# Kernel tuning notes

Measured on AMD Instinct MI355X. Metric: run time of the kernel, lower is better.

## Reference

```python
import jax, jax.numpy as jnp
import numpy as np

B, S, H = 2, 4096, 1024   # batch, seq, hidden_size
I = 512                    # moe_intermediate_size
E = 8                      # n_routed_experts
TOPK = 2                   # num_experts_per_tok
NGROUP = 2                 # n_group
TOPK_GROUP = 1             # topk_group
ROUTED_SCALE = 1.0         # routed_scaling_factor


def setup_inputs() -> dict:
    key = jax.random.key(0)
    ks = jax.random.split(key, 9)
    def w(k, shape, s=0.05):
        return jax.random.normal(k, shape, dtype=jnp.float32) * s
    return {
        "hidden_states": jax.random.normal(ks[0], (B, S, H), dtype=jnp.float32),
        "router_weight": w(ks[1], (E, H)),
        "correction_bias": w(ks[2], (E,)),
        "w_gate": w(ks[3], (E, H, I)),
        "w_up": w(ks[4], (E, H, I)),
        "w_down": w(ks[5], (E, I, H)),
        "sw_gate": w(ks[6], (H, I)),
        "sw_up": w(ks[7], (H, I)),
        "sw_down": w(ks[8], (I, H)),
    }


def _silu(x):
    return x * jax.nn.sigmoid(x)


def reference(hidden_states, router_weight, correction_bias,
              w_gate, w_up, w_down, sw_gate, sw_up, sw_down):
    b, s, h = hidden_states.shape
    x = hidden_states.reshape(-1, h)                       # [T, H]

    # ---- Glm4MoeTopkRouter (sigmoid scores + group top-k) ----
    logits = x @ router_weight.T                            # [T, E] (fp32)
    scores = jax.nn.sigmoid(logits)
    scores_for_choice = scores + correction_bias[None, :]
    e_per_g = E // NGROUP
    # group score = sum of top-2 biased scores within each group
    group_scores = jax.lax.top_k(
        scores_for_choice.reshape(-1, NGROUP, e_per_g), 2)[0].sum(-1)  # [T, G]
    group_idx = jax.lax.top_k(group_scores, TOPK_GROUP)[1]             # [T, Gk]
    group_mask = jax.nn.one_hot(group_idx, NGROUP, dtype=scores.dtype).sum(1)  # [T, G]
    score_mask = jnp.repeat(group_mask, e_per_g, axis=1)               # [T, E]
    masked = jnp.where(score_mask > 0, scores_for_choice, 0.0)
    topk_idx = jax.lax.top_k(masked, TOPK)[1]                          # [T, K]
    topk_w = jnp.take_along_axis(scores, topk_idx, axis=1)             # [T, K]
    topk_w = topk_w / (topk_w.sum(-1, keepdims=True) + 1e-20)          # norm_topk_prob
    topk_w = topk_w * ROUTED_SCALE

    # ---- routed experts: gated-SiLU MLP per expert, weighted combine ----
    # combine weights [T, E]: zero for unselected experts (exactly equals the
    # original per-expert gather/scatter sum)
    comb = (jax.nn.one_hot(topk_idx, E, dtype=x.dtype) * topk_w[..., None]).sum(1)
    g = jnp.einsum('th,ehi->tei', x, w_gate)               # [T, E, I]
    u = jnp.einsum('th,ehi->tei', x, w_up)
    y = jnp.einsum('tei,eih->teh', _silu(g) * u, w_down)   # [T, E, H]
    routed = jnp.einsum('teh,te->th', y, comb).reshape(b, s, h)

    # ---- shared experts on the residual ----
    shared = (_silu(hidden_states @ sw_gate) * (hidden_states @ sw_up)) @ sw_down
    return routed + shared
```

## Files before the change

### kernel.cpp

```cpp
#include <hip/hip_runtime.h>
#include <math.h>
#include <stdint.h>

#define T_TOK 8192
#define HDIM 1024
#define IDIM 512
#define NEXP 8
#define NGRP 2
#define EPG 4

typedef unsigned short u16;
typedef __attribute__((ext_vector_type(8))) short short8;
typedef __attribute__((ext_vector_type(4))) float f32x4;

#define GLD16(gp, lp) __builtin_amdgcn_global_load_lds(                        \
    (const __attribute__((address_space(1))) unsigned int*)(gp),               \
    (__attribute__((address_space(3))) unsigned int*)(lp), 16, 0, 0)

__device__ __forceinline__ u16 f2bf(float f) {
    unsigned int u = __float_as_uint(f);
    u += 0x7fffu + ((u >> 16) & 1u);
    return (u16)(u >> 16);
}
__device__ __forceinline__ float bf2f(u16 v) {
    return __uint_as_float(((unsigned int)v) << 16);
}

__global__ __launch_bounds__(256)
void prologue(const float* __restrict__ X,
              const float* __restrict__ Wr, const float* __restrict__ bias,
              u16* __restrict__ Xb, float* __restrict__ wpair, int* __restrict__ topk_ids,
              const float* __restrict__ wg,  const float* __restrict__ wu,
              const float* __restrict__ wdn, const float* __restrict__ swg,
              const float* __restrict__ swu, const float* __restrict__ swd,
              u16* __restrict__ wgT, u16* __restrict__ wuT, u16* __restrict__ wdnT,
              u16* __restrict__ swgT, u16* __restrict__ swuT, u16* __restrict__ swdT)
{
    __shared__ float tile[64][65];
    const int bid = blockIdx.x;

    if (bid < 2048) {
        int wave = threadIdx.x >> 6;
        int lane = threadIdx.x & 63;
        int t = bid * 4 + wave;

        float acc[NEXP];
#pragma unroll
        for (int e = 0; e < NEXP; ++e) acc[e] = 0.f;

        const float4* X4 = (const float4*)(X + (size_t)t * HDIM);
#pragma unroll
        for (int jj = 0; jj < 4; ++jj) {
            float4 xv = X4[lane + jj * 64];
            ushort4 bv;
            bv.x = f2bf(xv.x); bv.y = f2bf(xv.y); bv.z = f2bf(xv.z); bv.w = f2bf(xv.w);
            *(ushort4*)(Xb + (size_t)t * HDIM + (size_t)(lane + jj * 64) * 4) = bv;
#pragma unroll
            for (int e = 0; e < NEXP; ++e) {
                const float4* W4 = (const float4*)(Wr + (size_t)e * HDIM);
                float4 wv = W4[lane + jj * 64];
                acc[e] += xv.x * wv.x + xv.y * wv.y + xv.z * wv.z + xv.w * wv.w;
            }
        }
#pragma unroll
        for (int e = 0; e < NEXP; ++e) {
#pragma unroll
            for (int off = 32; off >= 1; off >>= 1)
                acc[e] += __shfl_xor(acc[e], off, 64);
        }

        if (lane == 0) {
            float s[NEXP], b[NEXP];
#pragma unroll
            for (int e = 0; e < NEXP; ++e) {
                s[e] = 1.f / (1.f + expf(-acc[e]));
                b[e] = s[e] + bias[e];
            }
            float gs[NGRP];
#pragma unroll
            for (int g = 0; g < NGRP; ++g) {
                float m1 = -1e30f, m2 = -1e30f;
#pragma unroll
                for (int j = 0; j < EPG; ++j) {
                    float v = b[g * EPG + j];
                    if (v > m1) { m2 = m1; m1 = v; }
                    else if (v > m2) { m2 = v; }
                }
                gs[g] = m1 + m2;
            }
            int bg = (gs[1] > gs[0]) ? 1 : 0;
            float masked[NEXP];
#pragma unroll
            for (int e = 0; e < NEXP; ++e)
                masked[e] = ((e >> 2) == bg) ? b[e] : 0.0f;
            int i0 = 0; float v0 = masked[0];
#pragma unroll
            for (int e = 1; e < NEXP; ++e)
                if (masked[e] > v0) { v0 = masked[e]; i0 = e; }
            int i1 = -1; float v1 = -1e30f;
#pragma unroll
            for (int e = 0; e < NEXP; ++e) {
                if (e == i0) continue;
                if (masked[e] > v1) { v1 = masked[e]; i1 = e; }
            }
            float w0 = s[i0], w1 = s[i1];
            float inv = 1.f / (w0 + w1 + 1e-20f);
            w0 *= inv; w1 *= inv;
            wpair[t * 2 + 0] = w0;
            wpair[t * 2 + 1] = w1;
            topk_ids[t] = i0 | (i1 << 8);
        }
        return;
    }

    int tb = bid - 2048;
    int m = tb >> 7;
    int i = tb & 127;
    const float* src; u16* dst; int R, C;
    const size_t EW = (size_t)HDIM * IDIM;
    if (m < 8)       { src = wg  + (size_t)m * EW;        dst = wgT  + (size_t)m * EW;        R = HDIM; C = IDIM; }
    else if (m < 16) { src = wu  + (size_t)(m - 8) * EW;  dst = wuT  + (size_t)(m - 8) * EW;  R = HDIM; C = IDIM; }
    else if (m < 24) { src = wdn + (size_t)(m - 16) * EW; dst = wdnT + (size_t)(m - 16) * EW; R = IDIM; C = HDIM; }
    else if (m == 24){ src = swg; dst = swgT; R = HDIM; C = IDIM; }
    else if (m == 25){ src = swu; dst = swuT; R = HDIM; C = IDIM; }
    else             { src = swd; dst = swdT; R = IDIM; C = HDIM; }
    int r0, c0;
    if (R == HDIM) { r0 = (i & 15) * 64; c0 = (i >> 4) * 64; }
    else           { r0 = (i & 7) * 64;  c0 = (i >> 3) * 64; }

    int t = threadIdx.x;
    int row = t >> 2;
#pragma unroll
    for (int j = 0; j < 4; ++j) {
        int c = ((t & 3) + j * 4) * 4;
        *(float4*)&tile[row][c] = *(const float4*)(src + (size_t)(r0 + row) * C + c0 + c);
    }
    __syncthreads();
    int c = t >> 2;
    int rchunk = (t & 3) * 16;
    __attribute__((aligned(16))) u16 pack[16];
#pragma unroll
    for (int k = 0; k < 16; ++k)
        pack[k] = f2bf(tile[rchunk + k][c]);
    uint4* d4 = (uint4*)(dst + (size_t)(c0 + c) * R + r0 + rchunk);
    d4[0] = *(uint4*)&pack[0];
    d4[1] = *(uint4*)&pack[8];
}

__global__ __launch_bounds__(256)
void build_lists(const int* __restrict__ topk_ids,
                 int* __restrict__ counts,
                 int* __restrict__ pair_id)
{
    const int e = blockIdx.x;
    const int tid = threadIdx.x;
    const int lane = tid & 63;
    const int wid = tid >> 6;
    __shared__ int wsum[4];
    __shared__ int rb;
    if (tid == 0) rb = 0;
    __syncthreads();

    int* dst = pair_id + e * T_TOK;
    for (int c0 = 0; c0 < T_TOK; c0 += 256) {
        int t = c0 + tid;
        int ids = topk_ids[t];
        bool m0 = (ids & 0xff) == e;
        bool m1 = ((ids >> 8) & 0xff) == e;
        unsigned long long b0 = __ballot(m0);
        unsigned long long b1 = __ballot(m1);
        int n0 = __popcll(b0);
        int n1 = __popcll(b1);
        if (lane == 0) wsum[wid] = n0 + n1;
        __syncthreads();
        int pre = 0, tot = 0;
#pragma unroll
        for (int w = 0; w < 4; ++w) {
            int v = wsum[w];
            if (w < wid) pre += v;
            tot += v;
        }
        int mybase = rb + pre;
        unsigned long long ltmask = (lane == 63) ? ~0ull >> 1 : ((1ull << lane) - 1);
        if (m0) dst[mybase + __popcll(b0 & ltmask)] = t * 2;
        if (m1) dst[mybase + n0 + __popcll(b1 & ltmask)] = t * 2 + 1;
        __syncthreads();
        if (tid == 0) rb += tot;
    }
    __syncthreads();
    if (tid == 0) counts[e] = rb;
}

__global__ __launch_bounds__(512)
void gateup_all(const u16* __restrict__ Xb,
                const u16* __restrict__ WgT, const u16* __restrict__ WuT,
                const u16* __restrict__ sWgT, const u16* __restrict__ sWuT,
                u16* __restrict__ hs,
                u16* __restrict__ hp,
                const int* __restrict__ counts,
                const int* __restrict__ pair_id)
{
    const int z = blockIdx.z;
    const bool SH = (z == 0);
    const int e = z - 1;
    const int nrows = SH ? T_TOK : counts[e];
    const int bm0 = blockIdx.y * 128;
    if (bm0 >= nrows) return;
    const int bn0 = blockIdx.x * 64;
    const u16* wgT = SH ? sWgT : WgT + (size_t)e * HDIM * IDIM;
    const u16* wuT = SH ? sWuT : WuT + (size_t)e * HDIM * IDIM;
    const int* plist = SH ? nullptr : (pair_id + e * T_TOK);
    u16* hout = SH ? hs : hp;

    int ebase = 0;
    if (!SH) {
#pragma unroll
        for (int i = 0; i < NEXP; ++i) ebase += (i < e) ? counts[i] : 0;
    }

    __shared__ __attribute__((aligned(16))) short As[128 * 64];
    __shared__ __attribute__((aligned(16))) short Bg[64 * 64];
    __shared__ __attribute__((aligned(16))) short Bu[64 * 64];

    const int tid = threadIdx.x;
    const int lane = tid & 63;
    const int wid = tid >> 6;

    const char* aptr[2];
#pragma unroll
    for (int i = 0; i < 2; ++i) {
        int g = wid * 2 + i;
        int r = g * 8 + (lane >> 3);
        int row = bm0 + r;
        int srow;
        if (SH) srow = row;
        else    srow = (row < nrows) ? (plist[row] >> 1) : 0;
        int cslot = ((lane & 7) ^ (r & 7)) * 8;
        aptr[i] = (const char*)(Xb + (size_t)srow * HDIM + cslot);
    }
    const char* bgptr; const char* buptr;
    {
        int r = wid * 8 + (lane >> 3);
        int nn = bn0 + r;
        int cslot = ((lane & 7) ^ (r & 7)) * 8;
        bgptr = (const char*)(wgT + (size_t)nn * HDIM + cslot);
        buptr = (const char*)(wuT + (size_t)nn * HDIM + cslot);
    }

    const int wm = wid & 3, wn = wid >> 2;
    const int m0 = wm * 32, n0 = wn * 32;
    const int lr = lane & 15, lg = lane >> 4;

    f32x4 accg[2][2] = {};
    f32x4 accu[2][2] = {};

    for (int k0 = 0; k0 < HDIM; k0 += 64) {
#pragma unroll
        for (int i = 0; i < 2; ++i) {
            GLD16(aptr[i], (char*)As + (wid * 2 + i) * 1024);
            aptr[i] += 128;
        }
        GLD16(bgptr, (char*)Bg + wid * 1024);
        GLD16(buptr, (char*)Bu + wid * 1024);
        bgptr += 128; buptr += 128;
        __syncthreads();
#pragma unroll
        for (int kk = 0; kk < 2; ++kk) {
            short8 af[2], bgf[2], buf_[2];
#pragma unroll
            for (int mf = 0; mf < 2; ++mf) {
                int row = m0 + mf * 16 + lr;
                int slot = (kk * 4 + lg) ^ (row & 7);
                af[mf] = *(const short8*)((const char*)As + row * 128 + slot * 16);
            }
#pragma unroll
            for (int nf = 0; nf < 2; ++nf) {
                int row = n0 + nf * 16 + lr;
                int slot = (kk * 4 + lg) ^ (row & 7);
                bgf[nf]  = *(const short8*)((const char*)Bg + row * 128 + slot * 16);
                buf_[nf] = *(const short8*)((const char*)Bu + row * 128 + slot * 16);
            }
#pragma unroll
            for (int mf = 0; mf < 2; ++mf)
#pragma unroll
                for (int nf = 0; nf < 2; ++nf) {
                    accg[mf][nf] = __builtin_amdgcn_mfma_f32_16x16x32_bf16(af[mf], bgf[nf],  accg[mf][nf], 0, 0, 0);
                    accu[mf][nf] = __builtin_amdgcn_mfma_f32_16x16x32_bf16(af[mf], buf_[nf], accu[mf][nf], 0, 0, 0);
                }
        }
        __syncthreads();
    }

#pragma unroll
    for (int mf = 0; mf < 2; ++mf) {
#pragma unroll
        for (int j = 0; j < 4; ++j) {
            int row = bm0 + m0 + mf * 16 + lg * 4 + j;
            if (row >= nrows) continue;
            int outrow = SH ? row : (ebase + row);
            u16* dst = hout + (size_t)outrow * IDIM + bn0 + n0 + lr;
#pragma unroll
            for (int nf = 0; nf < 2; ++nf) {
                float g = accg[mf][nf][j], u = accu[mf][nf][j];
                float sg = g / (1.f + __expf(-g));
                dst[nf * 16] = f2bf(sg * u);
            }
        }
    }
}

__global__ __launch_bounds__(512)
void down_routed(const u16* __restrict__ Hp,
                 const u16* __restrict__ WdT,
                 u16* __restrict__ y0,
                 u16* __restrict__ y1,
                 const float* __restrict__ wpair,
                 const int* __restrict__ counts,
                 const int* __restrict__ pair_id)
{
    const int e = blockIdx.z;
    const int nrows = counts[e];
    const int bm0 = blockIdx.y * 128;
    if (bm0 >= nrows) return;
    const int bn0 = blockIdx.x * 128;
    const u16* wdT = WdT + (size_t)e * HDIM * IDIM;
    const int* plist = pair_id + e * T_TOK;

    int ebase = 0;
#pragma unroll
    for (int i = 0; i < NEXP; ++i) ebase += (i < e) ? counts[i] : 0;

    __shared__ __attribute__((aligned(16))) short As[128 * 64];
    __shared__ __attribute__((aligned(16))) short Bs[128 * 64];

    const int tid = threadIdx.x;
    const int lane = tid & 63;
    const int wid = tid >> 6;

    const char* aptr[2]; const char* bptr[2];
#pragma unroll
    for (int i = 0; i < 2; ++i) {
        int g = wid * 2 + i;
        int r = g * 8 + (lane >> 3);
        int row = bm0 + r;
        int srow = ebase + ((row < nrows) ? row : 0);
        int cslot = ((lane & 7) ^ (r & 7)) * 8;
        aptr[i] = (const char*)(Hp + (size_t)srow * IDIM + cslot);
        bptr[i] = (const char*)(wdT + (size_t)(bn0 + r) * IDIM + cslot);
    }

    const int wm = wid & 3, wn = wid >> 2;
    const int m0 = wm * 32, n0 = wn * 64;
    const int lr = lane & 15, lg = lane >> 4;

    f32x4 acc[2][4] = {};

    for (int k0 = 0; k0 < IDIM; k0 += 64) {
#pragma unroll
        for (int i = 0; i < 2; ++i) {
            GLD16(aptr[i], (char*)As + (wid * 2 + i) * 1024);
            GLD16(bptr[i], (char*)Bs + (wid * 2 + i) * 1024);
            aptr[i] += 128; bptr[i] += 128;
        }
        __syncthreads();
#pragma unroll
        for (int kk = 0; kk < 2; ++kk) {
            short8 af[2], bf[4];
#pragma unroll
            for (int mf = 0; mf < 2; ++mf) {
                int row = m0 + mf * 16 + lr;
                int slot = (kk * 4 + lg) ^ (row & 7);
                af[mf] = *(const short8*)((const char*)As + row * 128 + slot * 16);
            }
#pragma unroll
            for (int nf = 0; nf < 4; ++nf) {
                int row = n0 + nf * 16 + lr;
                int slot = (kk * 4 + lg) ^ (row & 7);
                bf[nf] = *(const short8*)((const char*)Bs + row * 128 + slot * 16);
            }
#pragma unroll
            for (int mf = 0; mf < 2; ++mf)
#pragma unroll
                for (int nf = 0; nf < 4; ++nf)
                    acc[mf][nf] = __builtin_amdgcn_mfma_f32_16x16x32_bf16(af[mf], bf[nf], acc[mf][nf], 0, 0, 0);
        }
        __syncthreads();
    }

#pragma unroll
    for (int mf = 0; mf < 2; ++mf) {
#pragma unroll
        for (int j = 0; j < 4; ++j) {
            int row = bm0 + m0 + mf * 16 + lg * 4 + j;
            if (row >= nrows) continue;
            int p = plist[row];
            int t = p >> 1;
            float w = wpair[p];
            u16* dst = ((p & 1) ? y1 : y0) + (size_t)t * HDIM + bn0 + n0 + lr;
#pragma unroll
            for (int nf = 0; nf < 4; ++nf)
                dst[nf * 16] = f2bf(acc[mf][nf][j] * w);
        }
    }
}

__global__ __launch_bounds__(512)
void down_shared_combine(const u16* __restrict__ Hs,
                         const u16* __restrict__ swdT,
                         const u16* __restrict__ y0,
                         const u16* __restrict__ y1,
                         float* __restrict__ out)
{
    const int bm0 = blockIdx.y * 128;
    const int bn0 = blockIdx.x * 128;

    __shared__ __attribute__((aligned(16))) short As[128 * 64];
    __shared__ __attribute__((aligned(16))) short Bs[128 * 64];

    const int tid = threadIdx.x;
    const int lane = tid & 63;
    const int wid = tid >> 6;

    const char* aptr[2]; const char* bptr[2];
#pragma unroll
    for (int i = 0; i < 2; ++i) {
        int g = wid * 2 + i;
        int r = g * 8 + (lane >> 3);
        int cslot = ((lane & 7) ^ (r & 7)) * 8;
        aptr[i] = (const char*)(Hs + (size_t)(bm0 + r) * IDIM + cslot);
        bptr[i] = (const char*)(swdT + (size_t)(bn0 + r) * IDIM + cslot);
    }

    const int wm = wid & 3, wn = wid >> 2;
    const int m0 = wm * 32, n0 = wn * 64;
    const int lr = lane & 15, lg = lane >> 4;

    f32x4 acc[2][4] = {};

    for (int k0 = 0; k0 < IDIM; k0 += 64) {
#pragma unroll
        for (int i = 0; i < 2; ++i) {
            GLD16(aptr[i], (char*)As + (wid * 2 + i) * 1024);
            GLD16(bptr[i], (char*)Bs + (wid * 2 + i) * 1024);
            aptr[i] += 128; bptr[i] += 128;
        }
        __syncthreads();
#pragma unroll
        for (int kk = 0; kk < 2; ++kk) {
            short8 af[2], bf[4];
#pragma unroll
            for (int mf = 0; mf < 2; ++mf) {
                int row = m0 + mf * 16 + lr;
                int slot = (kk * 4 + lg) ^ (row & 7);
                af[mf] = *(const short8*)((const char*)As + row * 128 + slot * 16);
            }
#pragma unroll
            for (int nf = 0; nf < 4; ++nf) {
                int row = n0 + nf * 16 + lr;
                int slot = (kk * 4 + lg) ^ (row & 7);
                bf[nf] = *(const short8*)((const char*)Bs + row * 128 + slot * 16);
            }
#pragma unroll
            for (int mf = 0; mf < 2; ++mf)
#pragma unroll
                for (int nf = 0; nf < 4; ++nf)
                    acc[mf][nf] = __builtin_amdgcn_mfma_f32_16x16x32_bf16(af[mf], bf[nf], acc[mf][nf], 0, 0, 0);
        }
        __syncthreads();
    }

#pragma unroll
    for (int mf = 0; mf < 2; ++mf) {
#pragma unroll
        for (int j = 0; j < 4; ++j) {
            int t = bm0 + m0 + mf * 16 + lg * 4 + j;
            float* dst = out + (size_t)t * HDIM + bn0 + n0 + lr;
            const u16* y0src = y0 + (size_t)t * HDIM + bn0 + n0 + lr;
            const u16* y1src = y1 + (size_t)t * HDIM + bn0 + n0 + lr;
#pragma unroll
            for (int nf = 0; nf < 4; ++nf)
                dst[nf * 16] = acc[mf][nf][j] + bf2f(y0src[nf * 16]) + bf2f(y1src[nf * 16]);
        }
    }
}

extern "C" void kernel_launch(void* const* d_in, const int* in_sizes, int n_in,
                              void* d_out, int out_size, void* d_ws, size_t ws_size,
                              hipStream_t stream) {
    const float* X    = (const float*)d_in[0];
    const float* Wr   = (const float*)d_in[1];
    const float* bias = (const float*)d_in[2];
    const float* wg   = (const float*)d_in[3];
    const float* wu   = (const float*)d_in[4];
    const float* wdn  = (const float*)d_in[5];
    const float* swg  = (const float*)d_in[6];
    const float* swu  = (const float*)d_in[7];
    const float* swd  = (const float*)d_in[8];
    float* out = (float*)d_out;
    (void)in_sizes; (void)n_in; (void)out_size; (void)ws_size;

    char* ws = (char*)d_ws;
    const size_t MB = 1048576;
    int*   counts   = (int*)ws;
    float* wpair    = (float*)(ws + 4096);
    int*   pair_id  = (int*)(ws + 4096 + 65536);
    int*   topk_ids = (int*)(ws + 524288);
    u16* Xb   = (u16*)(ws + 1 * MB);
    u16* wgT  = (u16*)(ws + 17 * MB);
    u16* wuT  = (u16*)(ws + 25 * MB);
    u16* wdnT = (u16*)(ws + 33 * MB);
    u16* swgT = (u16*)(ws + 41 * MB);
    u16* swuT = (u16*)(ws + 42 * MB);
    u16* swdT = (u16*)(ws + 43 * MB);
    u16* hs   = (u16*)(ws + 44 * MB);
    u16* hp   = (u16*)(ws + 52 * MB);
    u16* y1   = Xb;
    u16* y0   = wgT;

    prologue<<<2048 + 27 * 128, 256, 0, stream>>>(
        X, Wr, bias, Xb, wpair, topk_ids,
        wg, wu, wdn, swg, swu, swd, wgT, wuT, wdnT, swgT, swuT, swdT);
    build_lists<<<NEXP, 256, 0, stream>>>(topk_ids, counts, pair_id);

    gateup_all<<<dim3(IDIM / 64, T_TOK / 128, NEXP + 1), 512, 0, stream>>>(
        Xb, wgT, wuT, swgT, swuT, hs, hp, counts, pair_id);

    down_routed<<<dim3(HDIM / 128, T_TOK / 128, NEXP), 512, 0, stream>>>(
        hp, wdnT, y0, y1, wpair, counts, pair_id);

    down_shared_combine<<<dim3(HDIM / 128, T_TOK / 128, 1), 512, 0, stream>>>(
        hs, swdT, y0, y1, out);
}
```

Measured before the change: 169.5 us.

## Merge shared down-proj into routed down kernel and add separate combine pass

The shared-expert down projection moves into the routed down kernel as an extra grid z-slice, so both GEMMs run in one launch and fill the GPU together instead of back to back. The shared slice writes fp32 partials straight to the output. A new vectorized elementwise kernel then adds the two bf16 routed outputs into the output buffer. This trades an extra read and write pass over the fp32 output for better occupancy and one fewer serialized GEMM launch.

```diff
diff --git a/kernel.cpp b/kernel.cpp
--- a/kernel.cpp
+++ b/kernel.cpp
@@ -310,25 +310,32 @@
 }
 
 __global__ __launch_bounds__(512)
-void down_routed(const u16* __restrict__ Hp,
-                 const u16* __restrict__ WdT,
-                 u16* __restrict__ y0,
-                 u16* __restrict__ y1,
-                 const float* __restrict__ wpair,
-                 const int* __restrict__ counts,
-                 const int* __restrict__ pair_id)
+void down_all(const u16* __restrict__ Hp,
+              const u16* __restrict__ Hs,
+              const u16* __restrict__ WdT,
+              const u16* __restrict__ swdT,
+              u16* __restrict__ y0,
+              u16* __restrict__ y1,
+              float* __restrict__ out,
+              const float* __restrict__ wpair,
+              const int* __restrict__ counts,
+              const int* __restrict__ pair_id)
 {
-    const int e = blockIdx.z;
-    const int nrows = counts[e];
+    const int z = blockIdx.z;
+    const bool SH = (z == NEXP);
+    const int e = z;
+    const int nrows = SH ? T_TOK : counts[e];
     const int bm0 = blockIdx.y * 128;
     if (bm0 >= nrows) return;
     const int bn0 = blockIdx.x * 128;
-    const u16* wdT = WdT + (size_t)e * HDIM * IDIM;
-    const int* plist = pair_id + e * T_TOK;
+    const u16* bsrc = SH ? swdT : WdT + (size_t)e * HDIM * IDIM;
+    const int* plist = SH ? nullptr : (pair_id + e * T_TOK);
 
     int ebase = 0;
-#pragma unroll
-    for (int i = 0; i < NEXP; ++i) ebase += (i < e) ? counts[i] : 0;
+    if (!SH) {
+#pragma unroll
+        for (int i = 0; i < NEXP; ++i) ebase += (i < e) ? counts[i] : 0;
+    }
 
     __shared__ __attribute__((aligned(16))) short As[128 * 64];
     __shared__ __attribute__((aligned(16))) short Bs[128 * 64];
@@ -343,10 +350,14 @@
         int g = wid * 2 + i;
         int r = g * 8 + (lane >> 3);
         int row = bm0 + r;
-        int srow = ebase + ((row < nrows) ? row : 0);
         int cslot = ((lane & 7) ^ (r & 7)) * 8;
-        aptr[i] = (const char*)(Hp + (size_t)srow * IDIM + cslot);
-        bptr[i] = (const char*)(wdT + (size_t)(bn0 + r) * IDIM + cslot);
+        if (SH) {
+            aptr[i] = (const char*)(Hs + (size_t)row * IDIM + cslot);
+        } else {
+            int srow = ebase + ((row < nrows) ? row : 0);
+            aptr[i] = (const char*)(Hp + (size_t)srow * IDIM + cslot);
+        }
+        bptr[i] = (const char*)(bsrc + (size_t)(bn0 + r) * IDIM + cslot);
     }
 
     const int wm = wid & 3, wn = wid >> 2;
@@ -393,95 +404,50 @@
         for (int j = 0; j < 4; ++j) {
             int row = bm0 + m0 + mf * 16 + lg * 4 + j;
             if (row >= nrows) continue;
-            int p = plist[row];
-            int t = p >> 1;
-            float w = wpair[p];
-            u16* dst = ((p & 1) ? y1 : y0) + (size_t)t * HDIM + bn0 + n0 + lr;
-#pragma unroll
-            for (int nf = 0; nf < 4; ++nf)
-                dst[nf * 16] = f2bf(acc[mf][nf][j] * w);
-        }
-    }
-}
-
-__global__ __launch_bounds__(512)
-void down_shared_combine(const u16* __restrict__ Hs,
-                         const u16* __restrict__ swdT,
-                         const u16* __restrict__ y0,
-                         const u16* __restrict__ y1,
-                         float* __restrict__ out)
+            if (SH) {
+                float* dst = out + (size_t)row * HDIM + bn0 + n0 + lr;
+#pragma unroll
+                for (int nf = 0; nf < 4; ++nf)
+                    dst[nf * 16] = acc[mf][nf][j];
+            } else {
+                int p = plist[row];
+                int t = p >> 1;
+                float w = wpair[p];
+                u16* dst = ((p & 1) ? y1 : y0) + (size_t)t * HDIM + bn0 + n0 + lr;
+#pragma unroll
+                for (int nf = 0; nf < 4; ++nf)
+                    dst[nf * 16] = f2bf(acc[mf][nf][j] * w);
+            }
+        }
+    }
+}
+
+__global__ __launch_bounds__(256)
+void combine(float* __restrict__ out,
+             const u16* __restrict__ y0,
+             const u16* __restrict__ y1)
 {
-    const int bm0 = blockIdx.y * 128;
-    const int bn0 = blockIdx.x * 128;
-
-    __shared__ __attribute__((aligned(16))) short As[128 * 64];
-    __shared__ __attribute__((aligned(16))) short Bs[128 * 64];
-
-    const int tid = threadIdx.x;
-    const int lane = tid & 63;
-    const int wid = tid >> 6;
-
-    const char* aptr[2]; const char* bptr[2];
-#pragma unroll
-    for (int i = 0; i < 2; ++i) {
-        int g = wid * 2 + i;
-        int r = g * 8 + (lane >> 3);
-        int cslot = ((lane & 7) ^ (r & 7)) * 8;
-        aptr[i] = (const char*)(Hs + (size_t)(bm0 + r) * IDIM + cslot);
-        bptr[i] = (const char*)(swdT + (size_t)(bn0 + r) * IDIM + cslot);
-    }
-
-    const int wm = wid & 3, wn = wid >> 2;
-    const int m0 = wm * 32, n0 = wn * 64;
-    const int lr = lane & 15, lg = lane >> 4;
-
-    f32x4 acc[2][4] = {};
-
-    for (int k0 = 0; k0 < IDIM; k0 += 64) {
-#pragma unroll
-        for (int i = 0; i < 2; ++i) {
-            GLD16(aptr[i], (char*)As + (wid * 2 + i) * 1024);
-            GLD16(bptr[i], (char*)Bs + (wid * 2 + i) * 1024);
-            aptr[i] += 128; bptr[i] += 128;
-        }
-        __syncthreads();
-#pragma unroll
-        for (int kk = 0; kk < 2; ++kk) {
-            short8 af[2], bf[4];
-#pragma unroll
-            for (int mf = 0; mf < 2; ++mf) {
-                int row = m0 + mf * 16 + lr;
-                int slot = (kk * 4 + lg) ^ (row & 7);
-                af[mf] = *(const short8*)((const char*)As + row * 128 + slot * 16);
-            }
-#pragma unroll
-            for (int nf = 0; nf < 4; ++nf) {
-                int row = n0 + nf * 16 + lr;
-                int slot = (kk * 4 + lg) ^ (row & 7);
-                bf[nf] = *(const short8*)((const char*)Bs + row * 128 + slot * 16);
-            }
-#pragma unroll
-            for (int mf = 0; mf < 2; ++mf)
-#pragma unroll
-                for (int nf = 0; nf < 4; ++nf)
-                    acc[mf][nf] = __builtin_amdgcn_mfma_f32_16x16x32_bf16(af[mf], bf[nf], acc[mf][nf], 0, 0, 0);
-        }
-        __syncthreads();
-    }
-
-#pragma unroll
-    for (int mf = 0; mf < 2; ++mf) {
-#pragma unroll
-        for (int j = 0; j < 4; ++j) {
-            int t = bm0 + m0 + mf * 16 + lg * 4 + j;
-            float* dst = out + (size_t)t * HDIM + bn0 + n0 + lr;
-            const u16* y0src = y0 + (size_t)t * HDIM + bn0 + n0 + lr;
-            const u16* y1src = y1 + (size_t)t * HDIM + bn0 + n0 + lr;
-#pragma unroll
-            for (int nf = 0; nf < 4; ++nf)
-                dst[nf * 16] = acc[mf][nf][j] + bf2f(y0src[nf * 16]) + bf2f(y1src[nf * 16]);
-        }
-    }
+    size_t i = ((size_t)blockIdx.x * 256 + threadIdx.x) * 8;
+    uint4 a0 = *(const uint4*)(y0 + i);
+    uint4 a1 = *(const uint4*)(y1 + i);
+    float4 o0 = *(float4*)(out + i);
+    float4 o1 = *(float4*)(out + i + 4);
+    const unsigned int* p0 = (const unsigned int*)&a0;
+    const unsigned int* p1 = (const unsigned int*)&a1;
+    float r[8];
+#pragma unroll
+    for (int k = 0; k < 4; ++k) {
+        float lo0 = __uint_as_float(p0[k] << 16);
+        float hi0 = __uint_as_float(p0[k] & 0xffff0000u);
+        float lo1 = __uint_as_float(p1[k] << 16);
+        float hi1 = __uint_as_float(p1[k] & 0xffff0000u);
+        r[2 * k + 0] = lo0 + lo1;
+        r[2 * k + 1] = hi0 + hi1;
+    }
+    o0.x += r[0]; o0.y += r[1]; o0.z += r[2]; o0.w += r[3];
+    o1.x += r[4]; o1.y += r[5]; o1.z += r[6]; o1.w += r[7];
+    *(float4*)(out + i)     = o0;
+    *(float4*)(out + i + 4) = o1;
 }
 
 extern "C" void kernel_launch(void* const* d_in, const int* in_sizes, int n_in,
@@ -525,9 +491,8 @@
     gateup_all<<<dim3(IDIM / 64, T_TOK / 128, NEXP + 1), 512, 0, stream>>>(
         Xb, wgT, wuT, swgT, swuT, hs, hp, counts, pair_id);
 
-    down_routed<<<dim3(HDIM / 128, T_TOK / 128, NEXP), 512, 0, stream>>>(
-        hp, wdnT, y0, y1, wpair, counts, pair_id);
-
-    down_shared_combine<<<dim3(HDIM / 128, T_TOK / 128, 1), 512, 0, stream>>>(
-        hs, swdT, y0, y1, out);
-}
+    down_all<<<dim3(HDIM / 128, T_TOK / 128, NEXP + 1), 512, 0, stream>>>(
+        hp, hs, wdnT, swdT, y0, y1, out, wpair, counts, pair_id);
+
+    combine<<<(T_TOK * HDIM) / (256 * 8), 256, 0, stream>>>(out, y0, y1);
+}
```

Result: slower. 179.7 us (+6.0%).
